# Performance work log

Hardware: AMD Instinct MI355X
Metric: run time of the kernel (lower is better)

Reference implementation:

```python
import jax, jax.numpy as jnp
import numpy as np

NEG_SLOPE = 0.2

def setup_inputs() -> dict:
    key = jax.random.key(0)
    k1, k2, k3, k4 = jax.random.split(key, 4)
    n, in_f, heads, hidden = 4096, 256, 4, 64
    h = jax.random.normal(k1, (n, in_f), dtype=jnp.float32)
    adj = jax.random.randint(k2, (n, n, 1), 0, 2) > 0
    adj = adj | jnp.eye(n, dtype=bool)[:, :, None]  # self-loops so every row has a neighbor
    W = jax.random.normal(k3, (heads * hidden, in_f), dtype=jnp.float32) * (1.0 / np.sqrt(in_f))
    attn_w = jax.random.normal(k4, (1, 2 * hidden), dtype=jnp.float32) * (1.0 / np.sqrt(2 * hidden))
    return {"h": h, "adj_mat": adj, "W": W, "attn_w": attn_w}

def reference(h, adj_mat, W, attn_w):
    n, in_f = h.shape
    heads = 4
    hidden = W.shape[0] // heads
    # g = linear(h).view(n, heads, hidden)
    g = (h @ W.T).reshape(n, heads, hidden)
    # attn([g_i, g_j]) == g_i @ a_l + g_j @ a_r  (exact decomposition of the concat linear)
    a_l = attn_w[0, :hidden]
    a_r = attn_w[0, hidden:]
    score_l = jnp.einsum('nhf,f->nh', g, a_l)  # [n, heads]
    score_r = jnp.einsum('nhf,f->nh', g, a_r)
    e = score_l[:, None, :] + score_r[None, :, :]  # [n, n, heads]
    e = jnp.where(e >= 0, e, NEG_SLOPE * e)       # LeakyReLU
    e = jnp.where(adj_mat, e, -jnp.inf)            # mask non-edges
    a = jax.nn.softmax(e, axis=1)                  # softmax over source nodes j
    # dropout is identity in eval mode
    attn_res = jnp.einsum('ijh,jhf->ihf', a, g)    # [n, heads, hidden]
    return attn_res.reshape(n, heads * hidden)      # is_concat=True
```

## Files before the change

kernel.cpp:

```cpp
#include <hip/hip_runtime.h>
#include <hip/hip_bf16.h>
#include <stdint.h>

#define NN    4096
#define INF_  256
#define HEADS 4
#define HID   64
#define OUTC  256
#define NEG   0.2f
#define L2E   1.44269504f

#define BI     32
#define JSPLIT 8
#define NJ     (NN / JSPLIT)

typedef short bf16x8 __attribute__((ext_vector_type(8)));
typedef float f32x4  __attribute__((ext_vector_type(4)));

__device__ __forceinline__ uint32_t ford(float x){
  uint32_t u = __float_as_uint(x);
  return (u & 0x80000000u) ? ~u : (u | 0x80000000u);
}
__device__ __forceinline__ float funord(uint32_t e){
  uint32_t u = (e & 0x80000000u) ? (e & 0x7fffffffu) : ~e;
  return __uint_as_float(u);
}
__device__ __forceinline__ ushort bf16u(float f){
  __hip_bfloat16 b = __float2bfloat16(f);
  return *reinterpret_cast<ushort*>(&b);
}

__device__ __forceinline__ uint32_t pack16(int4 v0, int4 v1, int4 v2, int4 v3){
  uint32_t b = 0;
  b |= (v0.x ? 0x0001u : 0u); b |= (v0.y ? 0x0002u : 0u);
  b |= (v0.z ? 0x0004u : 0u); b |= (v0.w ? 0x0008u : 0u);
  b |= (v1.x ? 0x0010u : 0u); b |= (v1.y ? 0x0020u : 0u);
  b |= (v1.z ? 0x0040u : 0u); b |= (v1.w ? 0x0080u : 0u);
  b |= (v2.x ? 0x0100u : 0u); b |= (v2.y ? 0x0200u : 0u);
  b |= (v2.z ? 0x0400u : 0u); b |= (v2.w ? 0x0800u : 0u);
  b |= (v3.x ? 0x1000u : 0u); b |= (v3.y ? 0x2000u : 0u);
  b |= (v3.z ? 0x4000u : 0u); b |= (v3.w ? 0x8000u : 0u);
  return b;
}

__launch_bounds__(256)
__global__ void k_prep(const int* __restrict__ adj, const float* __restrict__ hmat,
                       const float* __restrict__ W, const float* __restrict__ aw,
                       ushort* __restrict__ bmb, short* __restrict__ gT,
                       float* __restrict__ slT2, float* __restrict__ srT2,
                       uint32_t* __restrict__ srmax2){
  __shared__ float hsT[64][68];
  __shared__ float wsT[64][68];
  __shared__ float smax_l[16];
  int bid = blockIdx.x;
  int t   = threadIdx.x;

  if (bid >= 256){
    int row = (bid - 256) * 2;
    const int* p0 = adj + (size_t)row*NN + t*16;
    const int* p1 = p0 + NN;
    int4 a0 = *(const int4*)(p0);      int4 a1 = *(const int4*)(p0 + 4);
    int4 a2 = *(const int4*)(p0 + 8);  int4 a3 = *(const int4*)(p0 + 12);
    int4 b0 = *(const int4*)(p1);      int4 b1 = *(const int4*)(p1 + 4);
    int4 b2 = *(const int4*)(p1 + 8);  int4 b3 = *(const int4*)(p1 + 12);
    bmb[(size_t)row*256 + t]       = (ushort)pack16(a0, a1, a2, a3);
    bmb[(size_t)(row + 1)*256 + t] = (ushort)pack16(b0, b1, b2, b3);
    return;
  }

  int tx = t & 15, ty = t >> 4;
  int r0 = (bid & 63) * 64;
  int cb = bid >> 6;
  int c0 = cb * 64;
  float acc[4][4] = {};

  for (int k0 = 0; k0 < INF_; k0 += 64){
    int row = t >> 2, kc = (t & 3) * 16;
    #pragma unroll
    for (int u = 0; u < 4; u++){
      float4 v = *(const float4*)&hmat[(r0 + row)*INF_ + k0 + kc + 4*u];
      hsT[kc + 4*u + 0][row] = v.x;
      hsT[kc + 4*u + 1][row] = v.y;
      hsT[kc + 4*u + 2][row] = v.z;
      hsT[kc + 4*u + 3][row] = v.w;
    }
    #pragma unroll
    for (int u = 0; u < 4; u++){
      float4 v = *(const float4*)&W[(c0 + row)*INF_ + k0 + kc + 4*u];
      wsT[kc + 4*u + 0][row] = v.x;
      wsT[kc + 4*u + 1][row] = v.y;
      wsT[kc + 4*u + 2][row] = v.z;
      wsT[kc + 4*u + 3][row] = v.w;
    }
    __syncthreads();
    #pragma unroll 8
    for (int k = 0; k < 64; k++){
      float4 hv = *(const float4*)&hsT[k][ty*4];
      float4 wv = *(const float4*)&wsT[k][tx*4];
      float ha[4] = {hv.x, hv.y, hv.z, hv.w};
      float wa[4] = {wv.x, wv.y, wv.z, wv.w};
      #pragma unroll
      for (int a_ = 0; a_ < 4; a_++)
        #pragma unroll
        for (int b_ = 0; b_ < 4; b_++)
          acc[a_][b_] = fmaf(ha[a_], wa[b_], acc[a_][b_]);
    }
    __syncthreads();
  }

  float alv[4], arv[4];
  #pragma unroll
  for (int j = 0; j < 4; j++){ alv[j] = aw[tx*4 + j]; arv[j] = aw[64 + tx*4 + j]; }
  float rmax = -3.4e38f;
  #pragma unroll
  for (int qi = 0; qi < 4; qi++){
    int r = r0 + ty*4 + qi;
    float slp = 0.f, srp = 0.f;
    #pragma unroll
    for (int j = 0; j < 4; j++){
      slp = fmaf(acc[qi][j], alv[j], slp);
      srp = fmaf(acc[qi][j], arv[j], srp);
    }
    #pragma unroll
    for (int m = 1; m < 16; m <<= 1){
      slp += __shfl_xor(slp, m, 64);
      srp += __shfl_xor(srp, m, 64);
    }
    if (tx == 0){
      slT2[(size_t)cb*NN + r] = slp * L2E;
      srT2[(size_t)cb*NN + r] = srp * L2E;
      rmax = fmaxf(rmax, srp * L2E);
    }
  }
  if (tx == 0) smax_l[ty] = rmax;

  float* T = (float*)hsT;
  #pragma unroll
  for (int qi = 0; qi < 4; qi++)
    #pragma unroll
    for (int j = 0; j < 4; j++)
      T[(tx*4 + j)*65 + ty*4 + qi] = acc[qi][j];
  __syncthreads();
  if (t == 0){
    float m = smax_l[0];
    #pragma unroll
    for (int i = 1; i < 16; i++) m = fmaxf(m, smax_l[i]);
    atomicMax(srmax2 + cb, ford(m));
  }
  int c = t >> 2, rb = (t & 3) * 16;
  ushort u16[16];
  #pragma unroll
  for (int v = 0; v < 16; v++) u16[v] = bf16u(T[c*65 + rb + v]);
  *(uint4*)&gT[(size_t)(c0 + c)*NN + r0 + rb]     = *(uint4*)&u16[0];
  *(uint4*)&gT[(size_t)(c0 + c)*NN + r0 + rb + 8] = *(uint4*)&u16[8];
}

__launch_bounds__(256, 4)
__global__ void k_attn(const short* __restrict__ gT, const float* __restrict__ slT2,
                       const float* __restrict__ srT2, const uint32_t* __restrict__ srmax2,
                       const uint32_t* __restrict__ bm,
                       __hip_bfloat16* __restrict__ num_p, float* __restrict__ den_p){
  __shared__ uint32_t bmlds[32 * 18];
  __shared__ float    srs[4][512];
  int t  = threadIdx.x;
  int h  = t >> 6, l = t & 63;
  int lr = l & 15, lg = l >> 4;
  int i0 = blockIdx.x * BI;
  int jb = blockIdx.y * NJ;
  int js = blockIdx.y;

  {
    int jj = l * 8;
    *(float4*)&srs[h][jj]     = *(const float4*)&srT2[(size_t)h*NN + jb + jj];
    *(float4*)&srs[h][jj + 4] = *(const float4*)&srT2[(size_t)h*NN + jb + jj + 4];
    int r = t >> 3, wd = (t & 7) * 2;
    uint2 v = *(const uint2*)&bm[(size_t)(i0 + r)*128 + (jb >> 5) + wd];
    bmlds[r*18 + wd]     = v.x;
    bmlds[r*18 + wd + 1] = v.y;
  }

  float srmaxh = funord(srmax2[h]);
  float d1[2], cc[2];
  #pragma unroll
  for (int m = 0; m < 2; m++){
    float slv = slT2[(size_t)h*NN + i0 + m*16 + lr];
    float xx  = slv + srmaxh;
    float msh = fmaxf(xx, NEG * xx);
    d1[m] = slv - msh;
    cc[m] = (NEG - 1.0f) * msh;
  }
  __syncthreads();

  f32x4 acc[2][4] = {};
  f32x4 dacc[2]   = {};
  bf16x8 ones;
  #pragma unroll
  for (int q = 0; q < 8; q++) ones[q] = (short)0x3F80;

  const short* gTh = gT + (size_t)h*HID*NN;
  const short* bp[4];
  #pragma unroll
  for (int n = 0; n < 4; n++)
    bp[n] = gTh + (size_t)(n*16 + lr)*NN + jb + lg*8;

  bf16x8 Bb[2][4];
  #pragma unroll
  for (int n = 0; n < 4; n++){
    Bb[0][n] = *(const bf16x8*)(bp[n]);
    Bb[1][n] = *(const bf16x8*)(bp[n] + 32);
  }

  float4 s0c = *(const float4*)&srs[h][lg*8];
  float4 s1c = *(const float4*)&srs[h][lg*8 + 4];
  uint32_t w0c = bmlds[lr*18];
  uint32_t w1c = bmlds[(16 + lr)*18];

  #pragma unroll
  for (int s = 0; s < 16; s++){
    float4 s0n = s0c, s1n = s1c;
    uint32_t w0n = 0, w1n = 0;
    if (s < 15){
      s0n = *(const float4*)&srs[h][(s+1)*32 + lg*8];
      s1n = *(const float4*)&srs[h][(s+1)*32 + lg*8 + 4];
      w0n = bmlds[lr*18 + s + 1];
      w1n = bmlds[(16 + lr)*18 + s + 1];
    }
    float sr8[8] = {s0c.x, s0c.y, s0c.z, s0c.w, s1c.x, s1c.y, s1c.z, s1c.w};

    bf16x8 A[2];
    #pragma unroll
    for (int m = 0; m < 2; m++){
      uint32_t word = (m ? w1c : w0c) >> (lg*8);
      uint32_t pk[4];
      #pragma unroll
      for (int p = 0; p < 4; p++){
        float z0 = d1[m] + sr8[2*p];
        float z1 = d1[m] + sr8[2*p + 1];
        float v0 = __builtin_amdgcn_exp2f(fmaxf(z0, fmaf(NEG, z0, cc[m])));
        float v1 = __builtin_amdgcn_exp2f(fmaxf(z1, fmaf(NEG, z1, cc[m])));
        int m0 = (int)(word << (31 - 2*p)) >> 31;
        int m1 = (int)(word << (30 - 2*p)) >> 31;
        v0 = __uint_as_float(__float_as_uint(v0) & (uint32_t)m0);
        v1 = __uint_as_float(__float_as_uint(v1) & (uint32_t)m1);
        uint32_t u0 = __float_as_uint(v0) + 0x8000u;
        uint32_t u1 = __float_as_uint(v1) + 0x8000u;
        pk[p] = __builtin_amdgcn_perm(u1, u0, 0x07060302u);
      }
      A[m] = *(bf16x8*)pk;
    }

    __builtin_amdgcn_s_setprio(1);
    dacc[0] = __builtin_amdgcn_mfma_f32_16x16x32_bf16(A[0], ones, dacc[0], 0, 0, 0);
    #pragma unroll
    for (int n = 0; n < 4; n++)
      acc[0][n] = __builtin_amdgcn_mfma_f32_16x16x32_bf16(A[0], Bb[s & 1][n], acc[0][n], 0, 0, 0);
    dacc[1] = __builtin_amdgcn_mfma_f32_16x16x32_bf16(A[1], ones, dacc[1], 0, 0, 0);
    #pragma unroll
    for (int n = 0; n < 4; n++)
      acc[1][n] = __builtin_amdgcn_mfma_f32_16x16x32_bf16(A[1], Bb[s & 1][n], acc[1][n], 0, 0, 0);
    __builtin_amdgcn_s_setprio(0);

    if (s + 2 < 16){
      #pragma unroll
      for (int n = 0; n < 4; n++)
        Bb[s & 1][n] = *(const bf16x8*)(bp[n] + (s + 2)*32);
    }
    s0c = s0n; s1c = s1n; w0c = w0n; w1c = w1n;
  }

  #pragma unroll
  for (int m = 0; m < 2; m++)
    #pragma unroll
    for (int n = 0; n < 4; n++)
      #pragma unroll
      for (int r = 0; r < 4; r++)
        num_p[((size_t)js*NN + i0 + m*16 + lg*4 + r)*OUTC + h*HID + n*16 + lr] =
            __float2bfloat16(acc[m][n][r]);

  if (lr == 0)
    #pragma unroll
    for (int m = 0; m < 2; m++)
      #pragma unroll
      for (int r = 0; r < 4; r++)
        den_p[((size_t)js*4 + h)*NN + i0 + m*16 + lg*4 + r] = dacc[m][r];
}

__global__ void k_comb(const __hip_bfloat16* __restrict__ num_p,
                       const float* __restrict__ den_p, float* __restrict__ out){
  int t  = threadIdx.x;
  int r  = blockIdx.x*2 + (t >> 7);
  int c2 = (t & 127) * 2;
  int h  = c2 >> 6;
  float s0 = 0.f, s1 = 0.f, d = 0.f;
  #pragma unroll
  for (int js = 0; js < JSPLIT; js++){
    uint32_t u = *(const uint32_t*)&num_p[((size_t)js*NN + r)*OUTC + c2];
    s0 += __uint_as_float(u << 16);
    s1 += __uint_as_float(u & 0xffff0000u);
  }
  #pragma unroll
  for (int js = 0; js < JSPLIT; js++)
    d += den_p[((size_t)js*4 + h)*NN + r];
  float inv = 1.0f / d;
  *(float2*)&out[(size_t)r*OUTC + c2] = make_float2(s0*inv, s1*inv);
}

extern "C" void kernel_launch(void* const* d_in, const int* in_sizes, int n_in,
                              void* d_out, int out_size, void* d_ws, size_t ws_size,
                              hipStream_t stream){
  const float* hmat = (const float*)d_in[0];
  const int*   adj  = (const int*)d_in[1];
  const float* W    = (const float*)d_in[2];
  const float* aw   = (const float*)d_in[3];
  float* out = (float*)d_out;
  char*  ws  = (char*)d_ws;

  uint32_t* srmax2 = (uint32_t*)(ws);
  float*    slT2   = (float*)(ws + 1024);
  float*    srT2   = (float*)(ws + 66560);
  short*    gT     = (short*)(ws + 132096);
  float*    den_p  = (float*)(ws + 2229248);
  __hip_bfloat16* num_p = (__hip_bfloat16*)(ws + 2753536);
  uint32_t* bmask  = (uint32_t*)(ws + 19530752);

  hipMemsetAsync(ws, 0, 64, stream);
  hipLaunchKernelGGL(k_prep, dim3(2304), dim3(256), 0, stream,
                     adj, hmat, W, aw, (ushort*)bmask, gT, slT2, srT2, srmax2);
  hipLaunchKernelGGL(k_attn, dim3(NN/BI, JSPLIT), dim3(256), 0, stream,
                     gT, slT2, srT2, srmax2, bmask, num_p, den_p);
  hipLaunchKernelGGL(k_comb, dim3(NN/2), dim3(256), 0, stream, num_p, den_p, out);
}
```

Measured before the change: 68.51 us.

## Split attention j-range across two wave groups with LDS reduction

k_attn blocks grow from 256 to 512 threads. Each head now has two waves that each cover half of the block's 512-column j-range, so each wave runs 8 steps instead of 16. The two halves' numerator and denominator accumulators are combined through a new LDS buffer in two staged passes before one wave group writes the results. This is meant to add more waves for latency hiding and shorten per-wave serial work. In exchange it adds LDS traffic, several barriers, and a tighter launch-bounds register budget that risks register spilling.

```diff
diff --git a/kernel.cpp b/kernel.cpp
--- a/kernel.cpp
+++ b/kernel.cpp
@@ -155,28 +155,28 @@
   *(uint4*)&gT[(size_t)(c0 + c)*NN + r0 + rb + 8] = *(uint4*)&u16[8];
 }
 
-__launch_bounds__(256, 4)
+__launch_bounds__(512, 8)
 __global__ void k_attn(const short* __restrict__ gT, const float* __restrict__ slT2,
                        const float* __restrict__ srT2, const uint32_t* __restrict__ srmax2,
                        const uint32_t* __restrict__ bm,
                        __hip_bfloat16* __restrict__ num_p, float* __restrict__ den_p){
+  __shared__ float    srs[4][512];
   __shared__ uint32_t bmlds[32 * 18];
-  __shared__ float    srs[4][512];
+  __shared__ float    red[16][256];
   int t  = threadIdx.x;
-  int h  = t >> 6, l = t & 63;
+  int w  = t >> 6, l = t & 63;
+  int h  = w & 3, jh = w >> 2;
   int lr = l & 15, lg = l >> 4;
   int i0 = blockIdx.x * BI;
-  int jb = blockIdx.y * NJ;
   int js = blockIdx.y;
+  int jbB = js * NJ;
+  int jb  = jbB + jh * 256;
 
   {
-    int jj = l * 8;
-    *(float4*)&srs[h][jj]     = *(const float4*)&srT2[(size_t)h*NN + jb + jj];
-    *(float4*)&srs[h][jj + 4] = *(const float4*)&srT2[(size_t)h*NN + jb + jj + 4];
-    int r = t >> 3, wd = (t & 7) * 2;
-    uint2 v = *(const uint2*)&bm[(size_t)(i0 + r)*128 + (jb >> 5) + wd];
-    bmlds[r*18 + wd]     = v.x;
-    bmlds[r*18 + wd + 1] = v.y;
+    int hh = t >> 7, jj = (t & 127) * 4;
+    *(float4*)&srs[hh][jj] = *(const float4*)&srT2[(size_t)hh*NN + jbB + jj];
+    int r = t >> 4, wd = t & 15;
+    bmlds[r*18 + wd] = bm[(size_t)(i0 + r)*128 + (jbB >> 5) + wd];
   }
 
   float srmaxh = funord(srmax2[h]);
@@ -210,20 +210,20 @@
     Bb[1][n] = *(const bf16x8*)(bp[n] + 32);
   }
 
-  float4 s0c = *(const float4*)&srs[h][lg*8];
-  float4 s1c = *(const float4*)&srs[h][lg*8 + 4];
-  uint32_t w0c = bmlds[lr*18];
-  uint32_t w1c = bmlds[(16 + lr)*18];
-
-  #pragma unroll
-  for (int s = 0; s < 16; s++){
+  float4 s0c = *(const float4*)&srs[h][jh*256 + lg*8];
+  float4 s1c = *(const float4*)&srs[h][jh*256 + lg*8 + 4];
+  uint32_t w0c = bmlds[lr*18 + jh*8];
+  uint32_t w1c = bmlds[(16 + lr)*18 + jh*8];
+
+  #pragma unroll
+  for (int s = 0; s < 8; s++){
     float4 s0n = s0c, s1n = s1c;
     uint32_t w0n = 0, w1n = 0;
-    if (s < 15){
-      s0n = *(const float4*)&srs[h][(s+1)*32 + lg*8];
-      s1n = *(const float4*)&srs[h][(s+1)*32 + lg*8 + 4];
-      w0n = bmlds[lr*18 + s + 1];
-      w1n = bmlds[(16 + lr)*18 + s + 1];
+    if (s < 7){
+      s0n = *(const float4*)&srs[h][jh*256 + (s+1)*32 + lg*8];
+      s1n = *(const float4*)&srs[h][jh*256 + (s+1)*32 + lg*8 + 4];
+      w0n = bmlds[lr*18 + jh*8 + s + 1];
+      w1n = bmlds[(16 + lr)*18 + jh*8 + s + 1];
     }
     float sr8[8] = {s0c.x, s0c.y, s0c.z, s0c.w, s1c.x, s1c.y, s1c.z, s1c.w};
 
@@ -260,7 +260,7 @@
       acc[1][n] = __builtin_amdgcn_mfma_f32_16x16x32_bf16(A[1], Bb[s & 1][n], acc[1][n], 0, 0, 0);
     __builtin_amdgcn_s_setprio(0);
 
-    if (s + 2 < 16){
+    if (s + 2 < 8){
       #pragma unroll
       for (int n = 0; n < 4; n++)
         Bb[s & 1][n] = *(const bf16x8*)(bp[n] + (s + 2)*32);
@@ -268,21 +268,75 @@
     s0c = s0n; s1c = s1n; w0c = w0n; w1c = w1n;
   }
 
-  #pragma unroll
-  for (int m = 0; m < 2; m++)
-    #pragma unroll
-    for (int n = 0; n < 4; n++)
-      #pragma unroll
-      for (int r = 0; r < 4; r++)
-        num_p[((size_t)js*NN + i0 + m*16 + lg*4 + r)*OUTC + h*HID + n*16 + lr] =
-            __float2bfloat16(acc[m][n][r]);
-
-  if (lr == 0)
-    #pragma unroll
-    for (int m = 0; m < 2; m++)
-      #pragma unroll
-      for (int r = 0; r < 4; r++)
-        den_p[((size_t)js*4 + h)*NN + i0 + m*16 + lg*4 + r] = dacc[m][r];
+  __syncthreads();
+  float* dred = (float*)bmlds;
+  if (jh == 1){
+    #pragma unroll
+    for (int m = 0; m < 2; m++)
+      #pragma unroll
+      for (int n = 0; n < 2; n++)
+        #pragma unroll
+        for (int r = 0; r < 4; r++)
+          red[m*8 + n*4 + r][h*64 + l] = acc[m][n][r];
+    if (lr == 0)
+      #pragma unroll
+      for (int m = 0; m < 2; m++)
+        #pragma unroll
+        for (int r = 0; r < 4; r++)
+          dred[h*32 + m*16 + lg*4 + r] = dacc[m][r];
+  }
+  __syncthreads();
+  if (jh == 0){
+    #pragma unroll
+    for (int m = 0; m < 2; m++)
+      #pragma unroll
+      for (int n = 0; n < 2; n++)
+        #pragma unroll
+        for (int r = 0; r < 4; r++)
+          acc[m][n][r] += red[m*8 + n*4 + r][h*64 + l];
+    if (lr == 0)
+      #pragma unroll
+      for (int m = 0; m < 2; m++)
+        #pragma unroll
+        for (int r = 0; r < 4; r++)
+          dacc[m][r] += dred[h*32 + m*16 + lg*4 + r];
+  }
+  __syncthreads();
+  if (jh == 1){
+    #pragma unroll
+    for (int m = 0; m < 2; m++)
+      #pragma unroll
+      for (int n = 2; n < 4; n++)
+        #pragma unroll
+        for (int r = 0; r < 4; r++)
+          red[m*8 + (n-2)*4 + r][h*64 + l] = acc[m][n][r];
+  }
+  __syncthreads();
+  if (jh == 0){
+    #pragma unroll
+    for (int m = 0; m < 2; m++)
+      #pragma unroll
+      for (int n = 2; n < 4; n++)
+        #pragma unroll
+        for (int r = 0; r < 4; r++)
+          acc[m][n][r] += red[m*8 + (n-2)*4 + r][h*64 + l];
+
+    #pragma unroll
+    for (int m = 0; m < 2; m++)
+      #pragma unroll
+      for (int n = 0; n < 4; n++)
+        #pragma unroll
+        for (int r = 0; r < 4; r++)
+          num_p[((size_t)js*NN + i0 + m*16 + lg*4 + r)*OUTC + h*HID + n*16 + lr] =
+              __float2bfloat16(acc[m][n][r]);
+
+    if (lr == 0)
+      #pragma unroll
+      for (int m = 0; m < 2; m++)
+        #pragma unroll
+        for (int r = 0; r < 4; r++)
+          den_p[((size_t)js*4 + h)*NN + i0 + m*16 + lg*4 + r] = dacc[m][r];
+  }
 }
 
 __global__ void k_comb(const __hip_bfloat16* __restrict__ num_p,
@@ -326,7 +380,7 @@
   hipMemsetAsync(ws, 0, 64, stream);
   hipLaunchKernelGGL(k_prep, dim3(2304), dim3(256), 0, stream,
                      adj, hmat, W, aw, (ushort*)bmask, gT, slT2, srT2, srmax2);
-  hipLaunchKernelGGL(k_attn, dim3(NN/BI, JSPLIT), dim3(256), 0, stream,
+  hipLaunchKernelGGL(k_attn, dim3(NN/BI, JSPLIT), dim3(512), 0, stream,
                      gT, slT2, srT2, srmax2, bmask, num_p, den_p);
   hipLaunchKernelGGL(k_comb, dim3(NN/2), dim3(256), 0, stream, num_p, den_p, out);
 }
```

New measurement: 248.6 us. 263% more time.

## Factor leaky-ReLU exponent into per-row and per-column terms, removing inner-loop exp

Applied to the files above, without the earlier changes.

Splits exp(leakyrelu(sl_i+sr_j)-max) into two separable products: exp(sr_j) times a per-row factor on the positive side, and exp(0.2*sr_j) times another per-row factor on the negative side. The per-column exponentials are computed once per block and stored in LDS as bf16. Inside the loop the code then only selects between them with a packed 16-bit compare against exp(-sl_i) and masks by adjacency. This removes per-element exp2 and float math from the hot loop, but it doubles the MFMA count and accumulator registers (launch bounds drop from 4 to 3 blocks). It also adds bf16 rounding error in the branch choice and in the factored exponentials.

```diff
diff --git a/kernel.cpp b/kernel.cpp
--- a/kernel.cpp
+++ b/kernel.cpp
@@ -14,8 +14,10 @@
 #define JSPLIT 8
 #define NJ     (NN / JSPLIT)
 
-typedef short bf16x8 __attribute__((ext_vector_type(8)));
-typedef float f32x4  __attribute__((ext_vector_type(4)));
+typedef short  bf16x8 __attribute__((ext_vector_type(8)));
+typedef float  f32x4  __attribute__((ext_vector_type(4)));
+typedef unsigned short u16x2 __attribute__((ext_vector_type(2)));
+typedef short  s16x2 __attribute__((ext_vector_type(2)));
 
 __device__ __forceinline__ uint32_t ford(float x){
   uint32_t u = __float_as_uint(x);
@@ -155,13 +157,16 @@
   *(uint4*)&gT[(size_t)(c0 + c)*NN + r0 + rb + 8] = *(uint4*)&u16[8];
 }
 
-__launch_bounds__(256, 4)
+__launch_bounds__(256, 3)
 __global__ void k_attn(const short* __restrict__ gT, const float* __restrict__ slT2,
                        const float* __restrict__ srT2, const uint32_t* __restrict__ srmax2,
                        const uint32_t* __restrict__ bm,
                        __hip_bfloat16* __restrict__ num_p, float* __restrict__ den_p){
+  __shared__ uint32_t pelds[4][256];
+  __shared__ uint32_t qelds[4][256];
   __shared__ uint32_t bmlds[32 * 18];
-  __shared__ float    srs[4][512];
+  __shared__ float    e1t[4][32];
+  __shared__ float    e2t[4][32];
   int t  = threadIdx.x;
   int h  = t >> 6, l = t & 63;
   int lr = l & 15, lg = l >> 4;
@@ -169,30 +174,51 @@
   int jb = blockIdx.y * NJ;
   int js = blockIdx.y;
 
+  float srmaxh = funord(srmax2[h]);
+
   {
     int jj = l * 8;
-    *(float4*)&srs[h][jj]     = *(const float4*)&srT2[(size_t)h*NN + jb + jj];
-    *(float4*)&srs[h][jj + 4] = *(const float4*)&srT2[(size_t)h*NN + jb + jj + 4];
+    float4 v0 = *(const float4*)&srT2[(size_t)h*NN + jb + jj];
+    float4 v1 = *(const float4*)&srT2[(size_t)h*NN + jb + jj + 4];
+    float sv[8] = {v0.x, v0.y, v0.z, v0.w, v1.x, v1.y, v1.z, v1.w};
+    uint32_t pp[4], qq[4];
+    #pragma unroll
+    for (int q = 0; q < 4; q++){
+      float s0 = sv[2*q]     - srmaxh;
+      float s1 = sv[2*q + 1] - srmaxh;
+      uint32_t p0 = __float_as_uint(__builtin_amdgcn_exp2f(s0)) + 0x8000u;
+      uint32_t p1 = __float_as_uint(__builtin_amdgcn_exp2f(s1)) + 0x8000u;
+      pp[q] = __builtin_amdgcn_perm(p1, p0, 0x07060302u);
+      uint32_t q0 = __float_as_uint(__builtin_amdgcn_exp2f(NEG * s0)) + 0x8000u;
+      uint32_t q1 = __float_as_uint(__builtin_amdgcn_exp2f(NEG * s1)) + 0x8000u;
+      qq[q] = __builtin_amdgcn_perm(q1, q0, 0x07060302u);
+    }
+    *(uint4*)&pelds[h][l*4] = *(uint4*)pp;
+    *(uint4*)&qelds[h][l*4] = *(uint4*)qq;
     int r = t >> 3, wd = (t & 7) * 2;
     uint2 v = *(const uint2*)&bm[(size_t)(i0 + r)*128 + (jb >> 5) + wd];
     bmlds[r*18 + wd]     = v.x;
     bmlds[r*18 + wd + 1] = v.y;
   }
-
-  float srmaxh = funord(srmax2[h]);
-  float d1[2], cc[2];
+  if (t < 128){
+    int hh = t >> 5, row = t & 31;
+    float xr = slT2[(size_t)hh*NN + i0 + row] + funord(srmax2[hh]);
+    float mshr = fmaxf(xr, NEG * xr);
+    e1t[hh][row] = __builtin_amdgcn_exp2f(xr - mshr);
+    e2t[hh][row] = __builtin_amdgcn_exp2f(fmaf(NEG, xr, -mshr));
+  }
+  uint32_t Pt2[2];
   #pragma unroll
   for (int m = 0; m < 2; m++){
     float slv = slT2[(size_t)h*NN + i0 + m*16 + lr];
-    float xx  = slv + srmaxh;
-    float msh = fmaxf(xx, NEG * xx);
-    d1[m] = slv - msh;
-    cc[m] = (NEG - 1.0f) * msh;
+    float x   = slv + srmaxh;
+    uint32_t pt16 = (__float_as_uint(__builtin_amdgcn_exp2f(-x)) + 0x8000u) >> 16;
+    Pt2[m] = pt16 | (pt16 << 16);
   }
   __syncthreads();
 
-  f32x4 acc[2][4] = {};
-  f32x4 dacc[2]   = {};
+  f32x4 acc1[2][4] = {}, acc2[2][4] = {};
+  f32x4 dacc1[2] = {}, dacc2[2] = {};
   bf16x8 ones;
   #pragma unroll
   for (int q = 0; q < 8; q++) ones[q] = (short)0x3F80;
@@ -210,54 +236,58 @@
     Bb[1][n] = *(const bf16x8*)(bp[n] + 32);
   }
 
-  float4 s0c = *(const float4*)&srs[h][lg*8];
-  float4 s1c = *(const float4*)&srs[h][lg*8 + 4];
+  uint4 pec = *(const uint4*)&pelds[h][lg*4];
+  uint4 qec = *(const uint4*)&qelds[h][lg*4];
   uint32_t w0c = bmlds[lr*18];
   uint32_t w1c = bmlds[(16 + lr)*18];
 
   #pragma unroll
   for (int s = 0; s < 16; s++){
-    float4 s0n = s0c, s1n = s1c;
+    uint4 pen = pec, qen = qec;
     uint32_t w0n = 0, w1n = 0;
     if (s < 15){
-      s0n = *(const float4*)&srs[h][(s+1)*32 + lg*8];
-      s1n = *(const float4*)&srs[h][(s+1)*32 + lg*8 + 4];
+      pen = *(const uint4*)&pelds[h][(s+1)*16 + lg*4];
+      qen = *(const uint4*)&qelds[h][(s+1)*16 + lg*4];
       w0n = bmlds[lr*18 + s + 1];
       w1n = bmlds[(16 + lr)*18 + s + 1];
     }
-    float sr8[8] = {s0c.x, s0c.y, s0c.z, s0c.w, s1c.x, s1c.y, s1c.z, s1c.w};
-
-    bf16x8 A[2];
+    uint32_t pea[4] = {pec.x, pec.y, pec.z, pec.w};
+    uint32_t qea[4] = {qec.x, qec.y, qec.z, qec.w};
+
+    bf16x8 A1[2], A2[2];
     #pragma unroll
     for (int m = 0; m < 2; m++){
       uint32_t word = (m ? w1c : w0c) >> (lg*8);
-      uint32_t pk[4];
+      uint32_t a1p[4], a2p[4];
       #pragma unroll
       for (int p = 0; p < 4; p++){
-        float z0 = d1[m] + sr8[2*p];
-        float z1 = d1[m] + sr8[2*p + 1];
-        float v0 = __builtin_amdgcn_exp2f(fmaxf(z0, fmaf(NEG, z0, cc[m])));
-        float v1 = __builtin_amdgcn_exp2f(fmaxf(z1, fmaf(NEG, z1, cc[m])));
-        int m0 = (int)(word << (31 - 2*p)) >> 31;
-        int m1 = (int)(word << (30 - 2*p)) >> 31;
-        v0 = __uint_as_float(__float_as_uint(v0) & (uint32_t)m0);
-        v1 = __uint_as_float(__float_as_uint(v1) & (uint32_t)m1);
-        uint32_t u0 = __float_as_uint(v0) + 0x8000u;
-        uint32_t u1 = __float_as_uint(v1) + 0x8000u;
-        pk[p] = __builtin_amdgcn_perm(u1, u0, 0x07060302u);
+        int b0 = (int)(word << (31 - 2*p)) >> 31;
+        int b1 = (int)(word << (30 - 2*p)) >> 31;
+        uint32_t adjM = __builtin_amdgcn_perm((uint32_t)b1, (uint32_t)b0, 0x05040100u);
+        u16x2 pv = *(u16x2*)&pea[p];
+        u16x2 tv = pv - *(u16x2*)&Pt2[m];
+        s16x2 cm = (*(s16x2*)&tv) >> 15;
+        uint32_t cmn = *(uint32_t*)&cm;
+        uint32_t padj = pea[p] & adjM;
+        uint32_t qadj = qea[p] & adjM;
+        a1p[p] = padj & ~cmn;
+        a2p[p] = qadj &  cmn;
       }
-      A[m] = *(bf16x8*)pk;
+      A1[m] = *(bf16x8*)a1p;
+      A2[m] = *(bf16x8*)a2p;
     }
 
     __builtin_amdgcn_s_setprio(1);
-    dacc[0] = __builtin_amdgcn_mfma_f32_16x16x32_bf16(A[0], ones, dacc[0], 0, 0, 0);
-    #pragma unroll
-    for (int n = 0; n < 4; n++)
-      acc[0][n] = __builtin_amdgcn_mfma_f32_16x16x32_bf16(A[0], Bb[s & 1][n], acc[0][n], 0, 0, 0);
-    dacc[1] = __builtin_amdgcn_mfma_f32_16x16x32_bf16(A[1], ones, dacc[1], 0, 0, 0);
-    #pragma unroll
-    for (int n = 0; n < 4; n++)
-      acc[1][n] = __builtin_amdgcn_mfma_f32_16x16x32_bf16(A[1], Bb[s & 1][n], acc[1][n], 0, 0, 0);
+    #pragma unroll
+    for (int m = 0; m < 2; m++){
+      dacc1[m] = __builtin_amdgcn_mfma_f32_16x16x32_bf16(A1[m], ones, dacc1[m], 0, 0, 0);
+      dacc2[m] = __builtin_amdgcn_mfma_f32_16x16x32_bf16(A2[m], ones, dacc2[m], 0, 0, 0);
+      #pragma unroll
+      for (int n = 0; n < 4; n++){
+        acc1[m][n] = __builtin_amdgcn_mfma_f32_16x16x32_bf16(A1[m], Bb[s & 1][n], acc1[m][n], 0, 0, 0);
+        acc2[m][n] = __builtin_amdgcn_mfma_f32_16x16x32_bf16(A2[m], Bb[s & 1][n], acc2[m][n], 0, 0, 0);
+      }
+    }
     __builtin_amdgcn_s_setprio(0);
 
     if (s + 2 < 16){
@@ -265,24 +295,31 @@
       for (int n = 0; n < 4; n++)
         Bb[s & 1][n] = *(const bf16x8*)(bp[n] + (s + 2)*32);
     }
-    s0c = s0n; s1c = s1n; w0c = w0n; w1c = w1n;
-  }
-
-  #pragma unroll
-  for (int m = 0; m < 2; m++)
+    pec = pen; qec = qen; w0c = w0n; w1c = w1n;
+  }
+
+  #pragma unroll
+  for (int m = 0; m < 2; m++){
+    float e1v[4], e2v[4];
+    #pragma unroll
+    for (int r = 0; r < 4; r++){
+      e1v[r] = e1t[h][m*16 + lg*4 + r];
+      e2v[r] = e2t[h][m*16 + lg*4 + r];
+    }
     #pragma unroll
     for (int n = 0; n < 4; n++)
       #pragma unroll
+      for (int r = 0; r < 4; r++){
+        float f = fmaf(e1v[r], acc1[m][n][r], e2v[r] * acc2[m][n][r]);
+        num_p[((size_t)js*NN + i0 + m*16 + lg*4 + r)*OUTC + h*HID + n*16 + lr] =
+            __float2bfloat16(f);
+      }
+    if (lr == 0)
+      #pragma unroll
       for (int r = 0; r < 4; r++)
-        num_p[((size_t)js*NN + i0 + m*16 + lg*4 + r)*OUTC + h*HID + n*16 + lr] =
-            __float2bfloat16(acc[m][n][r]);
-
-  if (lr == 0)
-    #pragma unroll
-    for (int m = 0; m < 2; m++)
-      #pragma unroll
-      for (int r = 0; r < 4; r++)
-        den_p[((size_t)js*4 + h)*NN + i0 + m*16 + lg*4 + r] = dacc[m][r];
+        den_p[((size_t)js*4 + h)*NN + i0 + m*16 + lg*4 + r] =
+            fmaf(e1v[r], dacc1[m][r], e2v[r] * dacc2[m][r]);
+  }
 }
 
 __global__ void k_comb(const __hip_bfloat16* __restrict__ num_p,
```

After: 68.03 us. No clear change (-0.7%).

## Double i-tile per block and stage shared g tiles in LDS

Applied to the files above, without the earlier changes.

The attention kernel block grows from 32 to 64 destination rows and from 256 to 512 threads, with two waves per head each covering 32 rows. The g^T B-operand tiles are loaded cooperatively from global memory into double-buffered LDS, with a block barrier every step, so both row halves reuse one global load. This halves global B traffic per output row but adds 15 __syncthreads per block and more LDS use, which may reduce occupancy and latency hiding.

```diff
diff --git a/kernel.cpp b/kernel.cpp
--- a/kernel.cpp
+++ b/kernel.cpp
@@ -10,7 +10,7 @@
 #define NEG   0.2f
 #define L2E   1.44269504f
 
-#define BI     32
+#define BI     64
 #define JSPLIT 8
 #define NJ     (NN / JSPLIT)
 
@@ -155,26 +155,35 @@
   *(uint4*)&gT[(size_t)(c0 + c)*NN + r0 + rb + 8] = *(uint4*)&u16[8];
 }
 
-__launch_bounds__(256, 4)
+__launch_bounds__(512)
 __global__ void k_attn(const short* __restrict__ gT, const float* __restrict__ slT2,
                        const float* __restrict__ srT2, const uint32_t* __restrict__ srmax2,
                        const uint32_t* __restrict__ bm,
                        __hip_bfloat16* __restrict__ num_p, float* __restrict__ den_p){
-  __shared__ uint32_t bmlds[32 * 18];
   __shared__ float    srs[4][512];
+  __shared__ uint32_t bmlds[64 * 18];
+  __shared__ short    Bst[2][4*64*40];
   int t  = threadIdx.x;
-  int h  = t >> 6, l = t & 63;
+  int w  = t >> 6, l = t & 63;
+  int h  = w & 3, ihalf = w >> 2;
   int lr = l & 15, lg = l >> 4;
-  int i0 = blockIdx.x * BI;
+  int ib = blockIdx.x * BI;
+  int i0 = ib + ihalf * 32;
   int jb = blockIdx.y * NJ;
   int js = blockIdx.y;
 
+  int sh  = t >> 7;
+  int srw = (t >> 1) & 63;
+  int spt = t & 1;
+  const short* gsrc = gT + (size_t)(sh*HID + srw)*NN + jb + spt*16;
+  short* ldst0 = &Bst[0][sh*2560 + srw*40 + spt*16];
+  short* ldst1 = &Bst[1][sh*2560 + srw*40 + spt*16];
+
   {
-    int jj = l * 8;
-    *(float4*)&srs[h][jj]     = *(const float4*)&srT2[(size_t)h*NN + jb + jj];
-    *(float4*)&srs[h][jj + 4] = *(const float4*)&srT2[(size_t)h*NN + jb + jj + 4];
+    int hh = t >> 7, jj = (t & 127) * 4;
+    *(float4*)&srs[hh][jj] = *(const float4*)&srT2[(size_t)hh*NN + jb + jj];
     int r = t >> 3, wd = (t & 7) * 2;
-    uint2 v = *(const uint2*)&bm[(size_t)(i0 + r)*128 + (jb >> 5) + wd];
+    uint2 v = *(const uint2*)&bm[(size_t)(ib + r)*128 + (jb >> 5) + wd];
     bmlds[r*18 + wd]     = v.x;
     bmlds[r*18 + wd + 1] = v.y;
   }
@@ -189,6 +198,13 @@
     d1[m] = slv - msh;
     cc[m] = (NEG - 1.0f) * msh;
   }
+
+  {
+    uint4 g0 = *(const uint4*)(gsrc);
+    uint4 g1 = *(const uint4*)(gsrc + 8);
+    *(uint4*)(ldst0)     = g0;
+    *(uint4*)(ldst0 + 8) = g1;
+  }
   __syncthreads();
 
   f32x4 acc[2][4] = {};
@@ -197,33 +213,35 @@
   #pragma unroll
   for (int q = 0; q < 8; q++) ones[q] = (short)0x3F80;
 
-  const short* gTh = gT + (size_t)h*HID*NN;
-  const short* bp[4];
+  const short* brd0 = &Bst[0][h*2560 + lr*40 + lg*8];
+  const short* brd1 = &Bst[1][h*2560 + lr*40 + lg*8];
+
+  bf16x8 Bb[4];
   #pragma unroll
   for (int n = 0; n < 4; n++)
-    bp[n] = gTh + (size_t)(n*16 + lr)*NN + jb + lg*8;
-
-  bf16x8 Bb[2][4];
-  #pragma unroll
-  for (int n = 0; n < 4; n++){
-    Bb[0][n] = *(const bf16x8*)(bp[n]);
-    Bb[1][n] = *(const bf16x8*)(bp[n] + 32);
-  }
-
+    Bb[n] = *(const bf16x8*)(brd0 + n*640);
+
+  int rowl0 = (ihalf*32 + lr) * 18;
+  int rowl1 = (ihalf*32 + 16 + lr) * 18;
   float4 s0c = *(const float4*)&srs[h][lg*8];
   float4 s1c = *(const float4*)&srs[h][lg*8 + 4];
-  uint32_t w0c = bmlds[lr*18];
-  uint32_t w1c = bmlds[(16 + lr)*18];
+  uint32_t w0c = bmlds[rowl0];
+  uint32_t w1c = bmlds[rowl1];
 
   #pragma unroll
   for (int s = 0; s < 16; s++){
+    uint4 g0, g1;
+    if (s < 15){
+      g0 = *(const uint4*)(gsrc + (s+1)*32);
+      g1 = *(const uint4*)(gsrc + (s+1)*32 + 8);
+    }
     float4 s0n = s0c, s1n = s1c;
     uint32_t w0n = 0, w1n = 0;
     if (s < 15){
       s0n = *(const float4*)&srs[h][(s+1)*32 + lg*8];
       s1n = *(const float4*)&srs[h][(s+1)*32 + lg*8 + 4];
-      w0n = bmlds[lr*18 + s + 1];
-      w1n = bmlds[(16 + lr)*18 + s + 1];
+      w0n = bmlds[rowl0 + s + 1];
+      w1n = bmlds[rowl1 + s + 1];
     }
     float sr8[8] = {s0c.x, s0c.y, s0c.z, s0c.w, s1c.x, s1c.y, s1c.z, s1c.w};
 
@@ -253,17 +271,22 @@
     dacc[0] = __builtin_amdgcn_mfma_f32_16x16x32_bf16(A[0], ones, dacc[0], 0, 0, 0);
     #pragma unroll
     for (int n = 0; n < 4; n++)
-      acc[0][n] = __builtin_amdgcn_mfma_f32_16x16x32_bf16(A[0], Bb[s & 1][n], acc[0][n], 0, 0, 0);
+      acc[0][n] = __builtin_amdgcn_mfma_f32_16x16x32_bf16(A[0], Bb[n], acc[0][n], 0, 0, 0);
     dacc[1] = __builtin_amdgcn_mfma_f32_16x16x32_bf16(A[1], ones, dacc[1], 0, 0, 0);
     #pragma unroll
     for (int n = 0; n < 4; n++)
-      acc[1][n] = __builtin_amdgcn_mfma_f32_16x16x32_bf16(A[1], Bb[s & 1][n], acc[1][n], 0, 0, 0);
+      acc[1][n] = __builtin_amdgcn_mfma_f32_16x16x32_bf16(A[1], Bb[n], acc[1][n], 0, 0, 0);
     __builtin_amdgcn_s_setprio(0);
 
-    if (s + 2 < 16){
+    if (s < 15){
+      short* dst = ((s+1) & 1) ? ldst1 : ldst0;
+      *(uint4*)(dst)     = g0;
+      *(uint4*)(dst + 8) = g1;
+      __syncthreads();
+      const short* rd = ((s+1) & 1) ? brd1 : brd0;
       #pragma unroll
       for (int n = 0; n < 4; n++)
-        Bb[s & 1][n] = *(const bf16x8*)(bp[n] + (s + 2)*32);
+        Bb[n] = *(const bf16x8*)(rd + n*640);
     }
     s0c = s0n; s1c = s1n; w0c = w0n; w1c = w1n;
   }
@@ -326,7 +349,7 @@
   hipMemsetAsync(ws, 0, 64, stream);
   hipLaunchKernelGGL(k_prep, dim3(2304), dim3(256), 0, stream,
                      adj, hmat, W, aw, (ushort*)bmask, gT, slT2, srT2, srmax2);
-  hipLaunchKernelGGL(k_attn, dim3(NN/BI, JSPLIT), dim3(256), 0, stream,
+  hipLaunchKernelGGL(k_attn, dim3(NN/BI, JSPLIT), dim3(512), 0, stream,
                      gT, slT2, srT2, srmax2, bmask, num_p, den_p);
   hipLaunchKernelGGL(k_comb, dim3(NN/2), dim3(256), 0, stream, num_p, den_p, out);
 }
```

Measured after the change: 59.43 us. -13.3%, faster.
